# Kernel optimization log

Hardware: AMD Instinct MI355X
Metric: run time of the kernel (lower is better)

## Reference

```python
import jax, jax.numpy as jnp
import numpy as np

T, BS, IC, HC, LAYERS = 512, 256, 128, 256, 2


def setup_inputs() -> dict:
    key = jax.random.key(0)
    ks = jax.random.split(key, 8)
    d = {"x": jax.random.normal(ks[0], (T, BS, IC), dtype=jnp.float32)}
    ics = [IC, HC]
    k = 1
    for l in range(LAYERS):
        d["Wih%d" % l] = jax.random.normal(ks[k], (4 * HC, ics[l]), dtype=jnp.float32) * 0.05; k += 1
        d["Whh%d" % l] = jax.random.normal(ks[k], (4 * HC, HC), dtype=jnp.float32) * 0.05; k += 1
        d["bih%d" % l] = jnp.zeros((4 * HC,), jnp.float32)
        d["bhh%d" % l] = jnp.zeros((4 * HC,), jnp.float32)
        d["lw%d" % l] = jax.random.normal(ks[k], (1, HC), dtype=jnp.float32) * 0.05; k += 1
        d["lb%d" % l] = jnp.zeros((1,), jnp.float32)
    return d


def _ste_round(u):
    # straight-through estimator: round in fwd, identity grad in bwd
    return u + jax.lax.stop_gradient(jnp.round(u) - u)


def _lstm_cell(x, h, c, Wih, Whh, bih, bhh):
    gates = x @ Wih.T + bih + h @ Whh.T + bhh  # [bs, 4*HC]
    i, f, g, o = jnp.split(gates, 4, axis=-1)
    nc = jax.nn.sigmoid(f) * c + jax.nn.sigmoid(i) * jnp.tanh(g)
    nh = jax.nn.sigmoid(o) * jnp.tanh(nc)
    return nh, nc


def _forward(x, params):
    bs = x.shape[1]
    inp = x
    hs, cs = [], []
    # skip flags and delta_u persist across layers (as in the torch code)
    skip = jnp.zeros((bs,), bool)
    du = jnp.zeros((bs, 1), x.dtype)
    for (Wih, Whh, bih, bhh, lw, lb) in params:
        def step(carry, xt, Wih=Wih, Whh=Whh, bih=bih, bhh=bhh, lw=lw, lb=lb):
            h, c, u, skip, du = carry
            bu = _ste_round(u)  # [bs,1]
            # no-skip branch (identical math to the gathered torch version)
            ch, cc = _lstm_cell(xt, h, c, Wih, Whh, bih, bhh)
            nh_n = ch * bu
            nc_n = cc * bu
            du_n = jax.nn.sigmoid(nc_n @ lw.T + lb)
            nu_n = du_n * bu
            # skip branch
            nh_s = h * (1.0 - bu)
            nc_s = c * (1.0 - bu)
            nu_s = jnp.clip(u + du, 0.0, 1.0) * (1.0 - bu)
            m = skip[:, None]
            nh = jnp.where(m, nh_s, nh_n)
            nc = jnp.where(m, nc_s, nc_n)
            nu = jnp.where(m, nu_s, nu_n)
            ndu = jnp.where(m, du, du_n)
            # number of steps to keep skipping; ceil has zero grad so stop_gradient is exact
            n_skips = jnp.ceil(0.5 / jax.lax.stop_gradient(nu)) - 1.0
            nskip = n_skips[:, 0] > 0
            return (nh, nc, nu, nskip, ndu), nh

        carry0 = (jnp.zeros((bs, HC), x.dtype),
                  jnp.zeros((bs, HC), x.dtype),
                  jnp.ones((bs, 1), x.dtype),
                  skip, du)
        (h, c, u, skip, du), seq = jax.lax.scan(step, carry0, inp)
        inp = seq  # [T, bs, HC] feeds next layer
        hs.append(h)
        cs.append(c)
    return inp, jnp.stack(hs, 0), jnp.stack(cs, 0)


def reference(x, Wih0, Whh0, bih0, bhh0, lw0, lb0, Wih1, Whh1, bih1, bhh1, lw1, lb1):
    params = [(Wih0, Whh0, bih0, bhh0, lw0, lb0),
              (Wih1, Whh1, bih1, bhh1, lw1, lb1)]
    out, hs, cs = _forward(x, params)
    return out, hs, cs
```

## Files before the change

### kernel.cpp

```cpp
#include <hip/hip_runtime.h>

#define TSTEPS 512
#define BSZ 256
#define HCH 256

typedef _Float16 f16x8 __attribute__((ext_vector_type(8)));
typedef _Float16 f16x4 __attribute__((ext_vector_type(4)));
typedef float    f32x4 __attribute__((ext_vector_type(4)));

__device__ __forceinline__ float sigmoidf_(float v) { return 1.f / (1.f + expf(-v)); }
__device__ __forceinline__ unsigned pack2h(_Float16 a, _Float16 b) {
    union { _Float16 h[2]; unsigned u; } x; x.h[0] = a; x.h[1] = b; return x.u;
}

template<int IC>
__global__ __launch_bounds__(256, 1)
void skiplstm(const float* __restrict__ x,
              const float* __restrict__ Wih, const float* __restrict__ Whh,
              const float* __restrict__ bih, const float* __restrict__ bhh,
              const float* __restrict__ lw,  const float* __restrict__ lb,
              float* __restrict__ seq_out,
              float* __restrict__ hs_out, float* __restrict__ cs_out,
              unsigned* __restrict__ hG,
              double* __restrict__ part,
              float* __restrict__ skipdu,
              unsigned* __restrict__ flags,
              int first_layer)
{
    constexpr bool FIRST = (IC == 128);
    constexpr int K   = IC + HCH;
    constexpr int KP  = K + 8;
    constexpr int ICP = IC + 8;
    constexpr int KTX = IC / 32;
    constexpr int KTH = HCH / 32;
    constexpr int HS_BYTES = 2 * 16 * 264 * 2;
    constexpr int XS_BYTES = 2 * 16 * ICP * 2;
    constexpr int POOL = (HS_BYTES > XS_BYTES) ? HS_BYTES : XS_BYTES;

    __shared__ _Float16 Wh [64][KP];
    __shared__ _Float16 Wl_[64][KP];
    __shared__ float    BV[64];
    __shared__ __align__(16) char pool[POOL];

    _Float16 (*Hsh)[264] = (_Float16(*)[264])pool;
    _Float16 (*Hsl)[264] = (_Float16(*)[264])(pool + 16*264*2);
    float    (*G)[20]    = (float(*)[20])pool;
    _Float16 (*XSh)[ICP] = (_Float16(*)[ICP])pool;
    _Float16 (*XSl)[ICP] = (_Float16(*)[ICP])(pool + 16*ICP*2);

    const int tid   = threadIdx.x;
    const int bid   = blockIdx.x;
    const int btile = bid & 15;
    const int jtile = bid >> 4;
    const int lane  = tid & 63;
    const int g     = tid >> 6;
    const int n16   = lane & 15;
    const int lg    = lane >> 4;
    const int c_    = g * 16 + n16;
    const int row_c = tid >> 4;
    const int q     = tid & 15;
    const int J     = jtile * 16 + q;
    const int brow  = btile * 16 + row_c;
    const int r0    = btile * 16;

    unsigned* gfl    = flags + (FIRST ? 0 : 256) + btile * 16;
    unsigned* myflag = gfl + jtile;

    for (int i4 = tid; i4 < 64 * (K / 4); i4 += 256) {
        const int c = i4 / (K / 4);
        const int k = (i4 - c * (K / 4)) * 4;
        const int grow = (c >> 4) * HCH + jtile * 16 + (c & 15);
        const float4 v = (k < IC)
            ? *(const float4*)(Wih + (size_t)grow * IC  + k)
            : *(const float4*)(Whh + (size_t)grow * HCH + (k - IC));
        f16x4 hi, lo;
        hi[0] = (_Float16)v.x; lo[0] = (_Float16)(v.x - (float)hi[0]);
        hi[1] = (_Float16)v.y; lo[1] = (_Float16)(v.y - (float)hi[1]);
        hi[2] = (_Float16)v.z; lo[2] = (_Float16)(v.z - (float)hi[2]);
        hi[3] = (_Float16)v.w; lo[3] = (_Float16)(v.w - (float)hi[3]);
        *(f16x4*)&Wh [c][k] = hi;
        *(f16x4*)&Wl_[c][k] = lo;
    }
    if (tid < 64) {
        const int grow = (tid >> 4) * HCH + jtile * 16 + (tid & 15);
        BV[tid] = bih[grow] + bhh[grow];
    }

    const float lwv = lw[J];
    const float lbv = lb[0];
    float h_r = 0.f, c_r = 0.f, u_r = 1.f, du_r;
    int skip_r;
    if (FIRST) { du_r = 0.f; skip_r = 0; }
    else { du_r = skipdu[brow]; skip_r = (skipdu[BSZ + brow] > 0.5f) ? 1 : 0; }

    auto stage_x = [&](int t) {
        for (int i4 = tid; i4 < 16 * (IC / 4); i4 += 256) {
            const int row = i4 / (IC / 4);
            const int k   = (i4 - row * (IC / 4)) * 4;
            const float4 v = *(const float4*)(x + ((size_t)t * BSZ + r0 + row) * IC + k);
            f16x4 hi, lo;
            hi[0] = (_Float16)v.x; lo[0] = (_Float16)(v.x - (float)hi[0]);
            hi[1] = (_Float16)v.y; lo[1] = (_Float16)(v.y - (float)hi[1]);
            hi[2] = (_Float16)v.z; lo[2] = (_Float16)(v.z - (float)hi[2]);
            hi[3] = (_Float16)v.w; lo[3] = (_Float16)(v.w - (float)hi[3]);
            *(f16x4*)&XSh[row][k] = hi;
            *(f16x4*)&XSl[row][k] = lo;
        }
    };

    auto arrive = [&](unsigned val) {
        asm volatile("s_waitcnt vmcnt(0) lgkmcnt(0)" ::: "memory");
        __syncthreads();
        if (tid == 0)
            __hip_atomic_store(myflag, val, __ATOMIC_RELAXED, __HIP_MEMORY_SCOPE_AGENT);
    };
    auto wait_ = [&](unsigned val) {
        if (tid < 16)
            while (__hip_atomic_load(gfl + tid, __ATOMIC_RELAXED,
                                     __HIP_MEMORY_SCOPE_AGENT) < val)
                __builtin_amdgcn_s_sleep(1);
        __syncthreads();
        asm volatile("" ::: "memory");
    };

    f32x4 accA, accB;
    auto xmfma = [&]() {
        const float bv = BV[c_];
        accA = f32x4{bv, bv, bv, bv};
        accB = f32x4{0.f, 0.f, 0.f, 0.f};
        #pragma unroll
        for (int kt = 0; kt < KTX; ++kt) {
            const int ko = kt * 32 + lg * 8;
            const f16x8 ah = *(const f16x8*)&XSh[n16][ko];
            const f16x8 al = *(const f16x8*)&XSl[n16][ko];
            const f16x8 bh = *(const f16x8*)&Wh [c_][ko];
            const f16x8 bl = *(const f16x8*)&Wl_[c_][ko];
            accA = __builtin_amdgcn_mfma_f32_16x16x32_f16(ah, bh, accA, 0, 0, 0);
            accB = __builtin_amdgcn_mfma_f32_16x16x32_f16(al, bh, accB, 0, 0, 0);
            accB = __builtin_amdgcn_mfma_f32_16x16x32_f16(ah, bl, accB, 0, 0, 0);
        }
    };

    auto u_advance = [&](double ps) {
        double s = ps;
        s += __shfl_xor(s, 1); s += __shfl_xor(s, 2);
        s += __shfl_xor(s, 4); s += __shfl_xor(s, 8);
        const float du_n = sigmoidf_((float)(s + (double)lbv));
        const float bu_p = rintf(u_r);
        float nu, ndu;
        if (skip_r) { nu = fminf(fmaxf(u_r + du_r, 0.f), 1.f) * (1.f - bu_p); ndu = du_r; }
        else        { nu = du_n * bu_p; ndu = du_n; }
        u_r = nu; du_r = ndu;
        skip_r = (nu < 0.5f) ? 1 : 0;
    };

    if (!FIRST) stage_x(0);
    arrive(1);
    if (FIRST) { stage_x(0); __syncthreads(); }
    xmfma();
    wait_(1);

    for (int t = 0; t < TSTEPS; ++t) {
        const int par  = t & 1;
        const int rpar = par ^ 1;

        if (t == 0) {
            for (int i = tid; i < HS_BYTES / 4; i += 256) ((unsigned*)pool)[i] = 0u;
            __syncthreads();
        } else {
            const size_t hb = ((size_t)(rpar * 16 + btile)) * 2 * 2048;
            unsigned vh[8], vl[8];
            #pragma unroll
            for (int i = 0; i < 8; ++i) {
                vh[i] = __hip_atomic_load(hG + hb + tid + i * 256,
                                          __ATOMIC_RELAXED, __HIP_MEMORY_SCOPE_AGENT);
                vl[i] = __hip_atomic_load(hG + hb + 2048 + tid + i * 256,
                                          __ATOMIC_RELAXED, __HIP_MEMORY_SCOPE_AGENT);
            }
            const double ps = __hip_atomic_load(
                part + ((size_t)rpar * 16 + btile) * 256 + tid,
                __ATOMIC_RELAXED, __HIP_MEMORY_SCOPE_AGENT);
            #pragma unroll
            for (int i = 0; i < 8; ++i) {
                const int w = tid + i * 256;
                *(unsigned*)&Hsh[w >> 7][(w & 127) * 2] = vh[i];
                *(unsigned*)&Hsl[w >> 7][(w & 127) * 2] = vl[i];
            }
            u_advance(ps);
            __syncthreads();
        }

        f16x8 hfh[KTH], hfl[KTH];
        #pragma unroll
        for (int ht = 0; ht < KTH; ++ht) {
            hfh[ht] = *(const f16x8*)&Hsh[n16][ht * 32 + lg * 8];
            hfl[ht] = *(const f16x8*)&Hsl[n16][ht * 32 + lg * 8];
        }
        __syncthreads();

        #pragma unroll
        for (int ht = 0; ht < KTH; ++ht) {
            const int ko = IC + ht * 32 + lg * 8;
            const f16x8 bh = *(const f16x8*)&Wh [c_][ko];
            const f16x8 bl = *(const f16x8*)&Wl_[c_][ko];
            accA = __builtin_amdgcn_mfma_f32_16x16x32_f16(hfh[ht], bh, accA, 0, 0, 0);
            accB = __builtin_amdgcn_mfma_f32_16x16x32_f16(hfl[ht], bh, accB, 0, 0, 0);
            accB = __builtin_amdgcn_mfma_f32_16x16x32_f16(hfh[ht], bl, accB, 0, 0, 0);
        }
        {
            const f32x4 acc = accA + accB;
            *(f32x4*)&G[c_][lg * 4] = acc;
        }
        __syncthreads();

        const float bu  = rintf(u_r);
        const float omb = 1.f - bu;
        const float g0 = G[ 0 + q][row_c];
        const float g1 = G[16 + q][row_c];
        const float g2 = G[32 + q][row_c];
        const float g3 = G[48 + q][row_c];
        const float si = sigmoidf_(g0);
        const float sf = sigmoidf_(g1);
        const float tg = tanhf(g2);
        const float so = sigmoidf_(g3);
        const float cc_ = sf * c_r + si * tg;
        const float ch_ = so * tanhf(cc_);
        const float nc_n = cc_ * bu;
        const float nh_n = ch_ * bu;
        const float nh = skip_r ? h_r * omb : nh_n;
        const float nc = skip_r ? c_r * omb : nc_n;
        h_r = nh; c_r = nc;

        const _Float16 hh = (_Float16)nh;
        const _Float16 hl = (_Float16)(nh - (float)hh);
        const unsigned hbits = pack2h(hh, hl);
        const unsigned pbits = (unsigned)__shfl_xor((int)hbits, 1);
        const unsigned word  = (q & 1) ? ((pbits >> 16) | (hbits & 0xffff0000u))
                                       : ((hbits & 0xffffu) | (pbits << 16));
        const size_t wb = (((size_t)par * 16 + btile) * 2 + (q & 1)) * 2048
                        + (size_t)row_c * 128 + (J >> 1);
        __hip_atomic_store(hG + wb, word, __ATOMIC_RELAXED, __HIP_MEMORY_SCOPE_AGENT);

        double dd = (double)nc_n * (double)lwv;
        dd += __shfl_xor(dd, 1); dd += __shfl_xor(dd, 2);
        dd += __shfl_xor(dd, 4); dd += __shfl_xor(dd, 8);
        if (q == 0)
            __hip_atomic_store(part + ((size_t)par * 16 + btile) * 256 + row_c * 16 + jtile,
                               dd, __ATOMIC_RELAXED, __HIP_MEMORY_SCOPE_AGENT);
        __syncthreads();

        const bool more = (t + 1 < TSTEPS);
        if (!FIRST && more) stage_x(t + 1);
        arrive((unsigned)(t + 2));
        __builtin_nontemporal_store(nh, seq_out + ((size_t)t * BSZ + brow) * HCH + J);
        if (more) {
            if (FIRST) { stage_x(t + 1); __syncthreads(); }
            xmfma();
        }
        wait_((unsigned)(t + 2));
    }

    {
        const double ps = __hip_atomic_load(
            part + ((size_t)((TSTEPS - 1) & 1) * 16 + btile) * 256 + tid,
            __ATOMIC_RELAXED, __HIP_MEMORY_SCOPE_AGENT);
        u_advance(ps);
    }

    hs_out[(size_t)brow * HCH + J] = h_r;
    cs_out[(size_t)brow * HCH + J] = c_r;
    if (FIRST && jtile == 0 && q == 0) {
        skipdu[brow]       = du_r;
        skipdu[BSZ + brow] = skip_r ? 1.f : 0.f;
    }
}

extern "C" void kernel_launch(void* const* d_in, const int* in_sizes, int n_in,
                              void* d_out, int out_size, void* d_ws, size_t ws_size,
                              hipStream_t stream)
{
    (void)in_sizes; (void)n_in; (void)out_size; (void)ws_size;

    const float* x    = (const float*)d_in[0];
    const float* Wih0 = (const float*)d_in[1];
    const float* Whh0 = (const float*)d_in[2];
    const float* bih0 = (const float*)d_in[3];
    const float* bhh0 = (const float*)d_in[4];
    const float* lw0  = (const float*)d_in[5];
    const float* lb0  = (const float*)d_in[6];
    const float* Wih1 = (const float*)d_in[7];
    const float* Whh1 = (const float*)d_in[8];
    const float* bih1 = (const float*)d_in[9];
    const float* bhh1 = (const float*)d_in[10];
    const float* lw1  = (const float*)d_in[11];
    const float* lb1  = (const float*)d_in[12];

    float* out = (float*)d_out;
    float* seq = out;
    float* hs0 = out + (size_t)512 * 256 * 256;
    float* hs1 = hs0 + 256 * 256;
    float* cs0 = hs1 + 256 * 256;
    float* cs1 = cs0 + 256 * 256;

    char* ws = (char*)d_ws;
    unsigned* hG     = (unsigned*)ws;
    double*   part   = (double*)  (ws + 524288);
    float*    skipdu = (float*)   (ws + 524288 + 65536);
    unsigned* flags  = (unsigned*)(ws + 524288 + 65536 + 2048);

    hipMemsetAsync(flags, 0, 2 * 256 * sizeof(unsigned), stream);

    int one = 1, zero = 0;
    {
        void* args[] = { (void*)&x,   (void*)&Wih0, (void*)&Whh0, (void*)&bih0,
                         (void*)&bhh0,(void*)&lw0,  (void*)&lb0,  (void*)&seq,
                         (void*)&hs0, (void*)&cs0,  (void*)&hG,   (void*)&part,
                         (void*)&skipdu, (void*)&flags, (void*)&one };
        hipLaunchCooperativeKernel(reinterpret_cast<void*>(skiplstm<128>),
                                   dim3(256), dim3(256), args, 0, stream);
    }
    {
        const float* x1 = seq;
        void* args[] = { (void*)&x1,  (void*)&Wih1, (void*)&Whh1, (void*)&bih1,
                         (void*)&bhh1,(void*)&lw1,  (void*)&lb1,  (void*)&seq,
                         (void*)&hs1, (void*)&cs1,  (void*)&hG,   (void*)&part,
                         (void*)&skipdu, (void*)&flags, (void*)&zero };
        hipLaunchCooperativeKernel(reinterpret_cast<void*>(skiplstm<256>),
                                   dim3(256), dim3(256), args, 0, stream);
    }
}
```

Before: 4.471 ms.

## Store weights and hidden state in MFMA fragment order, load h directly to registers

Weights, x and the global hidden-state exchange buffer are rearranged into MFMA operand fragment order. Each lane can then load its h fragment from global memory with a 16-byte system-coherent load straight into registers, which removes the LDS staging and two block barriers per step. The x loads for the next step are issued early into registers and converted after the arrive, overlapping the global latency with the recurrent MFMA. The risks are the correctness of the new fragment index mapping, the inline asm cache-bypass load semantics, and higher register pressure.

Measured after the change: 3.951 ms. 1.13x faster.

```diff
diff --git a/kernel.cpp b/kernel.cpp
--- a/kernel.cpp
+++ b/kernel.cpp
@@ -5,12 +5,19 @@
 #define HCH 256
 
 typedef _Float16 f16x8 __attribute__((ext_vector_type(8)));
-typedef _Float16 f16x4 __attribute__((ext_vector_type(4)));
 typedef float    f32x4 __attribute__((ext_vector_type(4)));
+typedef unsigned u32x4 __attribute__((ext_vector_type(4)));
 
 __device__ __forceinline__ float sigmoidf_(float v) { return 1.f / (1.f + expf(-v)); }
+
 __device__ __forceinline__ unsigned pack2h(_Float16 a, _Float16 b) {
-    union { _Float16 h[2]; unsigned u; } x; x.h[0] = a; x.h[1] = b; return x.u;
+    union { _Float16 h[2]; unsigned u; } t; t.h[0] = a; t.h[1] = b; return t.u;
+}
+
+__device__ __forceinline__ u32x4 load16_agent(const unsigned* p) {
+    u32x4 r;
+    asm volatile("global_load_dwordx4 %0, %1, off sc0 sc1" : "=v"(r) : "v"(p));
+    return r;
 }
 
 template<int IC>
@@ -24,29 +31,23 @@
               unsigned* __restrict__ hG,
               double* __restrict__ part,
               float* __restrict__ skipdu,
-              unsigned* __restrict__ flags,
-              int first_layer)
+              unsigned* __restrict__ flags)
 {
     constexpr bool FIRST = (IC == 128);
-    constexpr int K   = IC + HCH;
-    constexpr int KP  = K + 8;
-    constexpr int ICP = IC + 8;
-    constexpr int KTX = IC / 32;
-    constexpr int KTH = HCH / 32;
-    constexpr int HS_BYTES = 2 * 16 * 264 * 2;
-    constexpr int XS_BYTES = 2 * 16 * ICP * 2;
-    constexpr int POOL = (HS_BYTES > XS_BYTES) ? HS_BYTES : XS_BYTES;
-
-    __shared__ _Float16 Wh [64][KP];
-    __shared__ _Float16 Wl_[64][KP];
-    __shared__ float    BV[64];
-    __shared__ __align__(16) char pool[POOL];
-
-    _Float16 (*Hsh)[264] = (_Float16(*)[264])pool;
-    _Float16 (*Hsl)[264] = (_Float16(*)[264])(pool + 16*264*2);
-    float    (*G)[20]    = (float(*)[20])pool;
-    _Float16 (*XSh)[ICP] = (_Float16(*)[ICP])pool;
-    _Float16 (*XSl)[ICP] = (_Float16(*)[ICP])(pool + 16*ICP*2);
+    constexpr int K    = IC + HCH;
+    constexpr int KT   = K / 32;
+    constexpr int KTX  = IC / 32;
+    constexpr int KTH  = HCH / 32;
+    constexpr int NWF  = KT * 256;
+    constexpr int NXF  = KTX * 64;
+    constexpr int NXFT = NXF / 256 ? NXF / 256 : 1;
+
+    __shared__ f16x8 WFh[NWF];
+    __shared__ f16x8 WFl[NWF];
+    __shared__ f16x8 XFh[NXF];
+    __shared__ f16x8 XFl[NXF];
+    __shared__ float G[64][17];
+    __shared__ float BV[64];
 
     const int tid   = threadIdx.x;
     const int bid   = blockIdx.x;
@@ -55,8 +56,6 @@
     const int lane  = tid & 63;
     const int g     = tid >> 6;
     const int n16   = lane & 15;
-    const int lg    = lane >> 4;
-    const int c_    = g * 16 + n16;
     const int row_c = tid >> 4;
     const int q     = tid & 15;
     const int J     = jtile * 16 + q;
@@ -66,24 +65,34 @@
     unsigned* gfl    = flags + (FIRST ? 0 : 256) + btile * 16;
     unsigned* myflag = gfl + jtile;
 
-    for (int i4 = tid; i4 < 64 * (K / 4); i4 += 256) {
-        const int c = i4 / (K / 4);
-        const int k = (i4 - c * (K / 4)) * 4;
-        const int grow = (c >> 4) * HCH + jtile * 16 + (c & 15);
-        const float4 v = (k < IC)
-            ? *(const float4*)(Wih + (size_t)grow * IC  + k)
-            : *(const float4*)(Whh + (size_t)grow * HCH + (k - IC));
-        f16x4 hi, lo;
-        hi[0] = (_Float16)v.x; lo[0] = (_Float16)(v.x - (float)hi[0]);
-        hi[1] = (_Float16)v.y; lo[1] = (_Float16)(v.y - (float)hi[1]);
-        hi[2] = (_Float16)v.z; lo[2] = (_Float16)(v.z - (float)hi[2]);
-        hi[3] = (_Float16)v.w; lo[3] = (_Float16)(v.w - (float)hi[3]);
-        *(f16x4*)&Wh [c][k] = hi;
-        *(f16x4*)&Wl_[c][k] = lo;
+    for (int f = tid; f < NWF; f += 256) {
+        const int kt = f >> 8;
+        const int rm = f & 255;
+        const int gg = rm >> 6;
+        const int ln = rm & 63;
+        const int grow = gg * HCH + jtile * 16 + (ln & 15);
+        const int k0   = kt * 32 + (ln >> 4) * 8;
+        const float* src = (k0 < IC) ? (Wih + (size_t)grow * IC + k0)
+                                     : (Whh + (size_t)grow * HCH + (k0 - IC));
+        const float4 a = *(const float4*)src;
+        const float4 b = *(const float4*)(src + 4);
+        const float vv[8] = {a.x, a.y, a.z, a.w, b.x, b.y, b.z, b.w};
+        f16x8 hv, lv;
+        #pragma unroll
+        for (int e = 0; e < 8; ++e) {
+            const _Float16 hi = (_Float16)vv[e];
+            hv[e] = hi; lv[e] = (_Float16)(vv[e] - (float)hi);
+        }
+        WFh[f] = hv; WFl[f] = lv;
     }
     if (tid < 64) {
         const int grow = (tid >> 4) * HCH + jtile * 16 + (tid & 15);
         BV[tid] = bih[grow] + bhh[grow];
+    }
+    {
+        unsigned* hz = hG + ((size_t)(16 + btile)) * 2 * 2048;
+        for (int i = tid; i < 4096; i += 256)
+            __hip_atomic_store(hz + i, 0u, __ATOMIC_RELAXED, __HIP_MEMORY_SCOPE_AGENT);
     }
 
     const float lwv = lw[J];
@@ -93,18 +102,31 @@
     if (FIRST) { du_r = 0.f; skip_r = 0; }
     else { du_r = skipdu[brow]; skip_r = (skipdu[BSZ + brow] > 0.5f) ? 1 : 0; }
 
-    auto stage_x = [&](int t) {
-        for (int i4 = tid; i4 < 16 * (IC / 4); i4 += 256) {
-            const int row = i4 / (IC / 4);
-            const int k   = (i4 - row * (IC / 4)) * 4;
-            const float4 v = *(const float4*)(x + ((size_t)t * BSZ + r0 + row) * IC + k);
-            f16x4 hi, lo;
-            hi[0] = (_Float16)v.x; lo[0] = (_Float16)(v.x - (float)hi[0]);
-            hi[1] = (_Float16)v.y; lo[1] = (_Float16)(v.y - (float)hi[1]);
-            hi[2] = (_Float16)v.z; lo[2] = (_Float16)(v.z - (float)hi[2]);
-            hi[3] = (_Float16)v.w; lo[3] = (_Float16)(v.w - (float)hi[3]);
-            *(f16x4*)&XSh[row][k] = hi;
-            *(f16x4*)&XSl[row][k] = lo;
+    float4 xr[NXFT][2];
+    auto xload = [&](int t) {
+        #pragma unroll
+        for (int s = 0; s < NXFT; ++s) {
+            const int f  = tid + s * 256;
+            const int kt = f >> 6, ln = f & 63;
+            const float* p = x + ((size_t)t * BSZ + r0 + (ln & 15)) * IC
+                               + kt * 32 + (ln >> 4) * 8;
+            xr[s][0] = *(const float4*)p;
+            xr[s][1] = *(const float4*)(p + 4);
+        }
+    };
+    auto xconvert = [&]() {
+        #pragma unroll
+        for (int s = 0; s < NXFT; ++s) {
+            const int f = tid + s * 256;
+            const float vv[8] = {xr[s][0].x, xr[s][0].y, xr[s][0].z, xr[s][0].w,
+                                 xr[s][1].x, xr[s][1].y, xr[s][1].z, xr[s][1].w};
+            f16x8 hv, lv;
+            #pragma unroll
+            for (int e = 0; e < 8; ++e) {
+                const _Float16 hi = (_Float16)vv[e];
+                hv[e] = hi; lv[e] = (_Float16)(vv[e] - (float)hi);
+            }
+            XFh[f] = hv; XFl[f] = lv;
         }
     };
 
@@ -125,16 +147,15 @@
 
     f32x4 accA, accB;
     auto xmfma = [&]() {
-        const float bv = BV[c_];
+        const float bv = BV[g * 16 + n16];
         accA = f32x4{bv, bv, bv, bv};
         accB = f32x4{0.f, 0.f, 0.f, 0.f};
         #pragma unroll
         for (int kt = 0; kt < KTX; ++kt) {
-            const int ko = kt * 32 + lg * 8;
-            const f16x8 ah = *(const f16x8*)&XSh[n16][ko];
-            const f16x8 al = *(const f16x8*)&XSl[n16][ko];
-            const f16x8 bh = *(const f16x8*)&Wh [c_][ko];
-            const f16x8 bl = *(const f16x8*)&Wl_[c_][ko];
+            const f16x8 ah = XFh[kt * 64 + lane];
+            const f16x8 al = XFl[kt * 64 + lane];
+            const f16x8 bh = WFh[(kt * 4 + g) * 64 + lane];
+            const f16x8 bl = WFl[(kt * 4 + g) * 64 + lane];
             accA = __builtin_amdgcn_mfma_f32_16x16x32_f16(ah, bh, accA, 0, 0, 0);
             accB = __builtin_amdgcn_mfma_f32_16x16x32_f16(al, bh, accB, 0, 0, 0);
             accB = __builtin_amdgcn_mfma_f32_16x16x32_f16(ah, bl, accB, 0, 0, 0);
@@ -154,9 +175,10 @@
         skip_r = (nu < 0.5f) ? 1 : 0;
     };
 
-    if (!FIRST) stage_x(0);
+    xload(0);
     arrive(1);
-    if (FIRST) { stage_x(0); __syncthreads(); }
+    xconvert();
+    __syncthreads();
     xmfma();
     wait_(1);
 
@@ -164,52 +186,42 @@
         const int par  = t & 1;
         const int rpar = par ^ 1;
 
-        if (t == 0) {
-            for (int i = tid; i < HS_BYTES / 4; i += 256) ((unsigned*)pool)[i] = 0u;
-            __syncthreads();
+        u32x4 fh[KTH], fl[KTH];
+        double ps = 0.0;
+        if (t > 0) {
+            const unsigned* b0 = hG + ((size_t)(rpar * 16 + btile)) * 2 * 2048;
+            const unsigned* b1 = b0 + 2048;
+            #pragma unroll
+            for (int ht = 0; ht < KTH; ++ht) {
+                fh[ht] = load16_agent(b0 + (ht * 64 + lane) * 4);
+                fl[ht] = load16_agent(b1 + (ht * 64 + lane) * 4);
+            }
+            ps = __hip_atomic_load(part + ((size_t)rpar * 16 + btile) * 256 + tid,
+                                   __ATOMIC_RELAXED, __HIP_MEMORY_SCOPE_AGENT);
         } else {
-            const size_t hb = ((size_t)(rpar * 16 + btile)) * 2 * 2048;
-            unsigned vh[8], vl[8];
             #pragma unroll
-            for (int i = 0; i < 8; ++i) {
-                vh[i] = __hip_atomic_load(hG + hb + tid + i * 256,
-                                          __ATOMIC_RELAXED, __HIP_MEMORY_SCOPE_AGENT);
-                vl[i] = __hip_atomic_load(hG + hb + 2048 + tid + i * 256,
-                                          __ATOMIC_RELAXED, __HIP_MEMORY_SCOPE_AGENT);
-            }
-            const double ps = __hip_atomic_load(
-                part + ((size_t)rpar * 16 + btile) * 256 + tid,
-                __ATOMIC_RELAXED, __HIP_MEMORY_SCOPE_AGENT);
-            #pragma unroll
-            for (int i = 0; i < 8; ++i) {
-                const int w = tid + i * 256;
-                *(unsigned*)&Hsh[w >> 7][(w & 127) * 2] = vh[i];
-                *(unsigned*)&Hsl[w >> 7][(w & 127) * 2] = vl[i];
-            }
-            u_advance(ps);
-            __syncthreads();
-        }
-
-        f16x8 hfh[KTH], hfl[KTH];
+            for (int ht = 0; ht < KTH; ++ht) { fh[ht] = u32x4{0,0,0,0}; fl[ht] = u32x4{0,0,0,0}; }
+        }
+        if (t + 1 < TSTEPS) xload(t + 1);
+        if (t > 0) u_advance(ps);
+
+        asm volatile("s_waitcnt vmcnt(0)" ::: "memory");
+        __builtin_amdgcn_sched_barrier(0);
         #pragma unroll
         for (int ht = 0; ht < KTH; ++ht) {
-            hfh[ht] = *(const f16x8*)&Hsh[n16][ht * 32 + lg * 8];
-            hfl[ht] = *(const f16x8*)&Hsl[n16][ht * 32 + lg * 8];
-        }
-        __syncthreads();
-
-        #pragma unroll
-        for (int ht = 0; ht < KTH; ++ht) {
-            const int ko = IC + ht * 32 + lg * 8;
-            const f16x8 bh = *(const f16x8*)&Wh [c_][ko];
-            const f16x8 bl = *(const f16x8*)&Wl_[c_][ko];
-            accA = __builtin_amdgcn_mfma_f32_16x16x32_f16(hfh[ht], bh, accA, 0, 0, 0);
-            accB = __builtin_amdgcn_mfma_f32_16x16x32_f16(hfl[ht], bh, accB, 0, 0, 0);
-            accB = __builtin_amdgcn_mfma_f32_16x16x32_f16(hfh[ht], bl, accB, 0, 0, 0);
+            const f16x8 ah = __builtin_bit_cast(f16x8, fh[ht]);
+            const f16x8 al = __builtin_bit_cast(f16x8, fl[ht]);
+            const f16x8 bh = WFh[((KTX + ht) * 4 + g) * 64 + lane];
+            const f16x8 bl = WFl[((KTX + ht) * 4 + g) * 64 + lane];
+            accA = __builtin_amdgcn_mfma_f32_16x16x32_f16(ah, bh, accA, 0, 0, 0);
+            accB = __builtin_amdgcn_mfma_f32_16x16x32_f16(al, bh, accB, 0, 0, 0);
+            accB = __builtin_amdgcn_mfma_f32_16x16x32_f16(ah, bl, accB, 0, 0, 0);
         }
         {
             const f32x4 acc = accA + accB;
-            *(f32x4*)&G[c_][lg * 4] = acc;
+            const int c_ = g * 16 + n16, lg4 = (lane >> 4) * 4;
+            #pragma unroll
+            for (int j = 0; j < 4; ++j) G[c_][lg4 + j] = acc[j];
         }
         __syncthreads();
 
@@ -237,9 +249,11 @@
         const unsigned pbits = (unsigned)__shfl_xor((int)hbits, 1);
         const unsigned word  = (q & 1) ? ((pbits >> 16) | (hbits & 0xffff0000u))
                                        : ((hbits & 0xffffu) | (pbits << 16));
-        const size_t wb = (((size_t)par * 16 + btile) * 2 + (q & 1)) * 2048
-                        + (size_t)row_c * 128 + (J >> 1);
-        __hip_atomic_store(hG + wb, word, __ATOMIC_RELAXED, __HIP_MEMORY_SCOPE_AGENT);
+        const int hc0 = J & ~1;
+        const int fr  = (hc0 >> 5) * 64 + ((hc0 >> 3) & 3) * 16 + row_c;
+        const int dw  = fr * 4 + ((hc0 & 7) >> 1);
+        __hip_atomic_store(hG + ((size_t)(par * 16 + btile) * 2 + (q & 1)) * 2048 + dw,
+                           word, __ATOMIC_RELAXED, __HIP_MEMORY_SCOPE_AGENT);
 
         double dd = (double)nc_n * (double)lwv;
         dd += __shfl_xor(dd, 1); dd += __shfl_xor(dd, 2);
@@ -247,14 +261,13 @@
         if (q == 0)
             __hip_atomic_store(part + ((size_t)par * 16 + btile) * 256 + row_c * 16 + jtile,
                                dd, __ATOMIC_RELAXED, __HIP_MEMORY_SCOPE_AGENT);
-        __syncthreads();
-
-        const bool more = (t + 1 < TSTEPS);
-        if (!FIRST && more) stage_x(t + 1);
+
         arrive((unsigned)(t + 2));
+
         __builtin_nontemporal_store(nh, seq_out + ((size_t)t * BSZ + brow) * HCH + J);
-        if (more) {
-            if (FIRST) { stage_x(t + 1); __syncthreads(); }
+        if (t + 1 < TSTEPS) {
+            xconvert();
+            __syncthreads();
             xmfma();
         }
         wait_((unsigned)(t + 2));
@@ -310,12 +323,11 @@
 
     hipMemsetAsync(flags, 0, 2 * 256 * sizeof(unsigned), stream);
 
-    int one = 1, zero = 0;
     {
         void* args[] = { (void*)&x,   (void*)&Wih0, (void*)&Whh0, (void*)&bih0,
                          (void*)&bhh0,(void*)&lw0,  (void*)&lb0,  (void*)&seq,
                          (void*)&hs0, (void*)&cs0,  (void*)&hG,   (void*)&part,
-                         (void*)&skipdu, (void*)&flags, (void*)&one };
+                         (void*)&skipdu, (void*)&flags };
         hipLaunchCooperativeKernel(reinterpret_cast<void*>(skiplstm<128>),
                                    dim3(256), dim3(256), args, 0, stream);
     }
@@ -324,7 +336,7 @@
         void* args[] = { (void*)&x1,  (void*)&Wih1, (void*)&Whh1, (void*)&bih1,
                          (void*)&bhh1,(void*)&lw1,  (void*)&lb1,  (void*)&seq,
                          (void*)&hs1, (void*)&cs1,  (void*)&hG,   (void*)&part,
-                         (void*)&skipdu, (void*)&flags, (void*)&zero };
+                         (void*)&skipdu, (void*)&flags };
         hipLaunchCooperativeKernel(reinterpret_cast<void*>(skiplstm<256>),
                                    dim3(256), dim3(256), args, 0, stream);
     }
```
